# Kernel optimization log

Measured on AMD Instinct MI355X. Metric: run time of the kernel, lower is better.

Reference implementation:

```python
import jax, jax.numpy as jnp
import numpy as np

N_HEADS = 16
N_EMBD = 1024

def setup_inputs() -> dict:
    key = jax.random.key(0)
    k1, k2, k3, k4, k5 = jax.random.split(key, 5)
    B, T, C = 4, 2048, N_EMBD
    x = jax.random.normal(k1, (B, T, C), dtype=jnp.float32)
    # Linear weights stored as [in, out] (equivalent math to torch's x @ W.T + b)
    W_attn = jax.random.normal(k2, (C, 3 * C), dtype=jnp.float32) * 0.02
    b_attn = jax.random.normal(k3, (3 * C,), dtype=jnp.float32) * 0.02
    W_proj = jax.random.normal(k4, (C, C), dtype=jnp.float32) * 0.02
    b_proj = jax.random.normal(k5, (C,), dtype=jnp.float32) * 0.02
    return {"x": x, "W_attn": W_attn, "b_attn": b_attn, "W_proj": W_proj, "b_proj": b_proj}

def reference(x, W_attn, b_attn, W_proj, b_proj):
    B, T, C = x.shape
    H = N_HEADS
    D = C // H
    scale = 1.0 / jnp.sqrt(jnp.asarray(D, dtype=x.dtype))
    # fused QKV projection
    qkv = x @ W_attn + b_attn                      # [B, T, 3C]
    q, k, v = jnp.split(qkv, 3, axis=-1)           # each [B, T, C]
    q = q.reshape(B, T, H, D)
    k = k.reshape(B, T, H, D)
    v = v.reshape(B, T, H, D)
    # non-causal SDPA
    scores = jnp.einsum('bqhd,bkhd->bhqk', q, k) * scale  # [B, H, T, T]
    attn = jax.nn.softmax(scores, axis=-1)
    y = jnp.einsum('bhqk,bkhd->bqhd', attn, v)     # [B, T, H, D]
    y = y.reshape(B, T, C)
    return y @ W_proj + b_proj
```

## Files before the change

### kernel.cpp

```cpp
#include <hip/hip_runtime.h>

typedef short s16x8 __attribute__((ext_vector_type(8)));
typedef short s16x4 __attribute__((ext_vector_type(4)));
typedef float f32x4 __attribute__((ext_vector_type(4)));

__device__ __forceinline__ unsigned short f2bf(float f) {
  unsigned u = __float_as_uint(f);
  u += 0x7fffu + ((u >> 16) & 1u);
  return (unsigned short)(u >> 16);
}
__device__ __forceinline__ float bf2f(unsigned short h) {
  return __uint_as_float(((unsigned)h) << 16);
}

__device__ __forceinline__ f32x4 mfma16_bf16(s16x4 a, s16x4 b, f32x4 c) {
#if __has_builtin(__builtin_amdgcn_mfma_f32_16x16x16bf16_1k)
  return __builtin_amdgcn_mfma_f32_16x16x16bf16_1k(a, b, c, 0, 0, 0);
#else
  asm volatile("v_mfma_f32_16x16x16_bf16 %0, %1, %2, %0" : "+v"(c) : "v"(a), "v"(b));
  return c;
#endif
}

#define GLOAD_LDS16(g, l)                                          \
  __builtin_amdgcn_global_load_lds(                                \
      (const __attribute__((address_space(1))) void*)(g),          \
      (__attribute__((address_space(3))) void*)(l), 16, 0, 0)


__global__ __launch_bounds__(256) void cvt_x_bf16(const float* __restrict__ in,
                                                  unsigned short* __restrict__ out) {
  int i = (blockIdx.x * 256 + threadIdx.x) * 4;
  float4 v = *(const float4*)(in + i);
  ushort4 o;
  o.x = f2bf(v.x); o.y = f2bf(v.y); o.z = f2bf(v.z); o.w = f2bf(v.w);
  *(ushort4*)(out + i) = o;
}

__global__ __launch_bounds__(256) void transpose_w(const float* __restrict__ W,
                                                   unsigned short* __restrict__ Wt,
                                                   int R, int C) {
  __shared__ float tile[32][33];
  int c0 = blockIdx.x * 32, r0 = blockIdx.y * 32;
  int x = threadIdx.x, ty = threadIdx.y;
  for (int yy = ty; yy < 32; yy += 8)
    tile[yy][x] = W[(size_t)(r0 + yy) * C + c0 + x];
  __syncthreads();
  for (int yy = ty; yy < 32; yy += 8)
    Wt[(size_t)(c0 + yy) * R + r0 + x] = f2bf(tile[x][yy]);
}

__global__ __launch_bounds__(256) void transpose_v(const unsigned short* __restrict__ qkv,
                                                   unsigned short* __restrict__ vt) {
  __shared__ unsigned short TT[32][72];
  const int bh = blockIdx.y;
  const int t0 = blockIdx.x * 32;
  const int b = bh >> 4, h = bh & 15;
  const int t = threadIdx.x;
  {
    int row = t >> 3, c8 = (t & 7) * 8;
    const unsigned short* src =
        qkv + (size_t)(b * 2048 + t0 + row) * 3072 + 2048 + h * 64 + c8;
    *(uint4*)&TT[row][c8] = *(const uint4*)src;
  }
  __syncthreads();
  {
    int drow = t >> 2, tc8 = (t & 3) * 8;
    uint4 val;
    unsigned short* vp = (unsigned short*)&val;
    for (int j = 0; j < 8; j++) vp[j] = TT[tc8 + j][drow];
    *(uint4*)(vt + (size_t)(bh * 64 + drow) * 2048 + t0 + tc8) = val;
  }
}


template <bool OUT_BF16>
__global__ __launch_bounds__(256) void gemm_bt(const unsigned short* __restrict__ A,
                                               const unsigned short* __restrict__ Bt,
                                               const float* __restrict__ bias,
                                               void* __restrict__ Cout,
                                               int M, int N, int K) {
  __shared__ __align__(16) unsigned short As[128 * 32];
  __shared__ __align__(16) unsigned short Bs[128 * 32];

  const int tid  = threadIdx.x;
  const int lane = tid & 63;
  const int w    = tid >> 6;
  const int lr   = lane & 15;
  const int quad = lane >> 4;
  const int wm   = (w >> 1) * 64;
  const int wn   = (w & 1) * 64;
  const int m0   = blockIdx.x * 128;
  const int n0   = blockIdx.y * 128;

  f32x4 acc[4][4];
  for (int i = 0; i < 4; i++)
    for (int j = 0; j < 4; j++)
      acc[i][j] = f32x4{0.f, 0.f, 0.f, 0.f};

  const int srow = tid >> 2;
  const int scb  = (tid & 3) * 8;
  const unsigned short* Ap = A  + (size_t)(m0 + srow) * K + scb;
  const unsigned short* Bp = Bt + (size_t)(n0 + srow) * K + scb;
  unsigned short* lA0 = As + w * 512;
  unsigned short* lA1 = As + 2048 + w * 512;
  unsigned short* lB0 = Bs + w * 512;
  unsigned short* lB1 = Bs + 2048 + w * 512;

  for (int kk = 0; kk < K; kk += 32) {
    __syncthreads();
    GLOAD_LDS16(Ap + kk, lA0);
    GLOAD_LDS16(Ap + (size_t)64 * K + kk, lA1);
    GLOAD_LDS16(Bp + kk, lB0);
    GLOAD_LDS16(Bp + (size_t)64 * K + kk, lB1);
    __syncthreads();

    s16x8 af[4], bf[4];
    for (int i = 0; i < 4; i++) af[i] = *(const s16x8*)&As[(wm + i * 16 + lr) * 32 + quad * 8];
    for (int j = 0; j < 4; j++) bf[j] = *(const s16x8*)&Bs[(wn + j * 16 + lr) * 32 + quad * 8];
    for (int i = 0; i < 4; i++)
      for (int j = 0; j < 4; j++)
        acc[i][j] = __builtin_amdgcn_mfma_f32_16x16x32_bf16(af[i], bf[j], acc[i][j], 0, 0, 0);
  }

  for (int j = 0; j < 4; j++) {
    int col = n0 + wn + j * 16 + lr;
    float bc = bias[col];
    for (int i = 0; i < 4; i++) {
      int rowb = m0 + wm + i * 16 + quad * 4;
      for (int r = 0; r < 4; r++) {
        float v = acc[i][j][r] + bc;
        if (OUT_BF16)
          ((unsigned short*)Cout)[(size_t)(rowb + r) * N + col] = f2bf(v);
        else
          ((float*)Cout)[(size_t)(rowb + r) * N + col] = v;
      }
    }
  }
}


__global__ __launch_bounds__(256, 4) void attn_flash(const unsigned short* __restrict__ qkv,
                                                     const unsigned short* __restrict__ vt,
                                                     unsigned short* __restrict__ y) {
  const int T = 2048, C3 = 3072;
  const int bh = blockIdx.x & 63;
  const int qt = blockIdx.x >> 6;
  const int b  = bh >> 4;
  const int h  = bh & 15;
  const int q0 = qt * 128;

  const int tid  = threadIdx.x;
  const int lane = tid & 63;
  const int w    = tid >> 6;
  const int lr   = lane & 15;
  const int quad = lane >> 4;

  __shared__ __align__(16) unsigned short Ks[64][64];
  __shared__ __align__(16) unsigned short Vs[64][64];

  s16x8 qf[2][2];
  const float QSC = 0.18033688f;
  for (int j = 0; j < 2; j++)
    for (int c = 0; c < 2; c++) {
      const unsigned short* qp =
          qkv + (size_t)(b * T + q0 + w * 32 + j * 16 + lr) * C3 + h * 64 + c * 32 + quad * 8;
      s16x8 t = *(const s16x8*)qp;
      s16x8 o;
      for (int e = 0; e < 8; e++)
        o[e] = (short)f2bf(bf2f((unsigned short)t[e]) * QSC);
      qf[j][c] = o;
    }

  f32x4 O[2][4];
  for (int j = 0; j < 2; j++)
    for (int dt = 0; dt < 4; dt++) O[j][dt] = f32x4{0.f, 0.f, 0.f, 0.f};
  float l[2] = {0.f, 0.f};

  const int srow = tid >> 3;
  const int sc8  = (tid & 7) * 8;
  const int scb  = sc8 * 2;
  const unsigned short* kbase = qkv + (size_t)(b * T) * C3 + 1024 + (size_t)h * 64;
  const unsigned short* vbase = vt + (size_t)(bh * 64) * 2048;
  char* KsB = (char*)Ks;
  char* VsB = (char*)Vs;
  const int rswz = (lr & 7) << 4;

  for (int kt = 0; kt < 32; kt++) {
    const int k0 = kt * 64;
    __syncthreads();
    for (int rr = 0; rr < 64; rr += 32) {
      int row = srow + rr;
      int sw  = scb ^ ((row & 7) << 4);
      *(uint4*)(KsB + row * 128 + sw) =
          *(const uint4*)(kbase + (size_t)(k0 + row) * C3 + sc8);
      *(uint4*)(VsB + row * 128 + sw) =
          *(const uint4*)(vbase + (size_t)row * 2048 + k0 + sc8);
    }
    __syncthreads();

    for (int i = 0; i < 4; i++) {
      const char* krow = KsB + (i * 16 + lr) * 128;
      s16x8 kf0 = *(const s16x8*)(krow + ((quad * 16) ^ rswz));
      s16x8 kf1 = *(const s16x8*)(krow + ((64 + quad * 16) ^ rswz));
      s16x4 vf[4];
      for (int dt = 0; dt < 4; dt++)
        vf[dt] = *(const s16x4*)(VsB + (dt * 16 + lr) * 128 + ((i * 32 + quad * 8) ^ rswz));

      for (int j = 0; j < 2; j++) {
        f32x4 S = f32x4{0.f, 0.f, 0.f, 0.f};
        S = __builtin_amdgcn_mfma_f32_16x16x32_bf16(kf0, qf[j][0], S, 0, 0, 0);
        S = __builtin_amdgcn_mfma_f32_16x16x32_bf16(kf1, qf[j][1], S, 0, 0, 0);
        float p0 = __builtin_amdgcn_exp2f(S[0]);
        float p1 = __builtin_amdgcn_exp2f(S[1]);
        float p2 = __builtin_amdgcn_exp2f(S[2]);
        float p3 = __builtin_amdgcn_exp2f(S[3]);
        l[j] += (p0 + p1) + (p2 + p3);
        unsigned u0 = __float_as_uint(p0) + 0x8000u;
        unsigned u1 = __float_as_uint(p1) + 0x8000u;
        unsigned u2 = __float_as_uint(p2) + 0x8000u;
        unsigned u3 = __float_as_uint(p3) + 0x8000u;
        union { unsigned u[2]; s16x4 v; } pk;
        pk.u[0] = __builtin_amdgcn_perm(u1, u0, 0x07060302u);
        pk.u[1] = __builtin_amdgcn_perm(u3, u2, 0x07060302u);
        for (int dt = 0; dt < 4; dt++)
          O[j][dt] = mfma16_bf16(pk.v, vf[dt], O[j][dt]);
      }
    }
  }

  for (int j = 0; j < 2; j++) {
    float s = l[j];
    s += __shfl_xor(s, 16, 64);
    s += __shfl_xor(s, 32, 64);
    l[j] = 1.f / s;
  }
  for (int j = 0; j < 2; j++) {
    float inv[4];
    for (int r = 0; r < 4; r++) inv[r] = __shfl(l[j], quad * 4 + r, 64);
    for (int dt = 0; dt < 4; dt++) {
      int col = h * 64 + dt * 16 + lr;
      for (int r = 0; r < 4; r++) {
        int row = b * T + q0 + w * 32 + j * 16 + quad * 4 + r;
        y[(size_t)row * 1024 + col] = f2bf(O[j][dt][r] * inv[r]);
      }
    }
  }
}


extern "C" void kernel_launch(void* const* d_in, const int* in_sizes, int n_in,
                              void* d_out, int out_size, void* d_ws, size_t ws_size,
                              hipStream_t stream) {
  const float* x  = (const float*)d_in[0];
  const float* Wa = (const float*)d_in[1];
  const float* ba = (const float*)d_in[2];
  const float* Wp = (const float*)d_in[3];
  const float* bp = (const float*)d_in[4];
  float* out = (float*)d_out;

  char* ws = (char*)d_ws;
  unsigned short* xb  = (unsigned short*)ws;
  unsigned short* Wat = (unsigned short*)(ws + 16777216);
  unsigned short* Wpt = (unsigned short*)(ws + 23068672);
  unsigned short* qkv = (unsigned short*)(ws + 25165824);
  unsigned short* vtr = (unsigned short*)(ws + 75497472);

  cvt_x_bf16<<<8192, 256, 0, stream>>>(x, xb);
  transpose_w<<<dim3(96, 32), dim3(32, 8), 0, stream>>>(Wa, Wat, 1024, 3072);
  transpose_w<<<dim3(32, 32), dim3(32, 8), 0, stream>>>(Wp, Wpt, 1024, 1024);

  gemm_bt<true><<<dim3(64, 24), 256, 0, stream>>>(xb, Wat, ba, qkv, 8192, 3072, 1024);

  transpose_v<<<dim3(64, 64), 256, 0, stream>>>(qkv, vtr);

  attn_flash<<<1024, 256, 0, stream>>>(qkv, vtr, xb);

  gemm_bt<false><<<dim3(64, 8), 256, 0, stream>>>(xb, Wpt, bp, out, 8192, 1024, 1024);
}
```

Baseline: 291.6 us.

## Use 16x16x32 MFMA for PV and compute row sums via MFMA with ones

```diff
diff --git a/kernel.cpp b/kernel.cpp
--- a/kernel.cpp
+++ b/kernel.cpp
@@ -11,15 +11,6 @@
 }
 __device__ __forceinline__ float bf2f(unsigned short h) {
   return __uint_as_float(((unsigned)h) << 16);
-}
-
-__device__ __forceinline__ f32x4 mfma16_bf16(s16x4 a, s16x4 b, f32x4 c) {
-#if __has_builtin(__builtin_amdgcn_mfma_f32_16x16x16bf16_1k)
-  return __builtin_amdgcn_mfma_f32_16x16x16bf16_1k(a, b, c, 0, 0, 0);
-#else
-  asm volatile("v_mfma_f32_16x16x16_bf16 %0, %1, %2, %0" : "+v"(c) : "v"(a), "v"(b));
-  return c;
-#endif
 }
 
 #define GLOAD_LDS16(g, l)                                          \
@@ -172,10 +163,15 @@
       qf[j][c] = o;
     }
 
+  s16x8 ones;
+  for (int e = 0; e < 8; e++) ones[e] = (short)0x3F80;
+
   f32x4 O[2][4];
-  for (int j = 0; j < 2; j++)
+  f32x4 Lacc[2];
+  for (int j = 0; j < 2; j++) {
     for (int dt = 0; dt < 4; dt++) O[j][dt] = f32x4{0.f, 0.f, 0.f, 0.f};
-  float l[2] = {0.f, 0.f};
+    Lacc[j] = f32x4{0.f, 0.f, 0.f, 0.f};
+  }
 
   const int srow = tid >> 3;
   const int sc8  = (tid & 7) * 8;
@@ -191,58 +187,61 @@
     __syncthreads();
     for (int rr = 0; rr < 64; rr += 32) {
       int row = srow + rr;
+      int r32 = row & 31;
+      int key = (row & ~31) | (((r32 & 12) << 1) | ((r32 >> 4) << 2) | (r32 & 3));
       int sw  = scb ^ ((row & 7) << 4);
       *(uint4*)(KsB + row * 128 + sw) =
-          *(const uint4*)(kbase + (size_t)(k0 + row) * C3 + sc8);
+          *(const uint4*)(kbase + (size_t)(k0 + key) * C3 + sc8);
       *(uint4*)(VsB + row * 128 + sw) =
           *(const uint4*)(vbase + (size_t)row * 2048 + k0 + sc8);
     }
     __syncthreads();
 
-    for (int i = 0; i < 4; i++) {
-      const char* krow = KsB + (i * 16 + lr) * 128;
-      s16x8 kf0 = *(const s16x8*)(krow + ((quad * 16) ^ rswz));
-      s16x8 kf1 = *(const s16x8*)(krow + ((64 + quad * 16) ^ rswz));
-      s16x4 vf[4];
+    for (int ch = 0; ch < 2; ch++) {
+      const char* krowA = KsB + (ch * 32 + lr) * 128;
+      const char* krowB = KsB + (ch * 32 + 16 + lr) * 128;
+      s16x8 kA0 = *(const s16x8*)(krowA + ((quad * 16) ^ rswz));
+      s16x8 kA1 = *(const s16x8*)(krowA + ((64 + quad * 16) ^ rswz));
+      s16x8 kB0 = *(const s16x8*)(krowB + ((quad * 16) ^ rswz));
+      s16x8 kB1 = *(const s16x8*)(krowB + ((64 + quad * 16) ^ rswz));
+      s16x8 vf[4];
       for (int dt = 0; dt < 4; dt++)
-        vf[dt] = *(const s16x4*)(VsB + (dt * 16 + lr) * 128 + ((i * 32 + quad * 8) ^ rswz));
+        vf[dt] = *(const s16x8*)(VsB + (dt * 16 + lr) * 128 + ((ch * 64 + quad * 16) ^ rswz));
 
       for (int j = 0; j < 2; j++) {
-        f32x4 S = f32x4{0.f, 0.f, 0.f, 0.f};
-        S = __builtin_amdgcn_mfma_f32_16x16x32_bf16(kf0, qf[j][0], S, 0, 0, 0);
-        S = __builtin_amdgcn_mfma_f32_16x16x32_bf16(kf1, qf[j][1], S, 0, 0, 0);
-        float p0 = __builtin_amdgcn_exp2f(S[0]);
-        float p1 = __builtin_amdgcn_exp2f(S[1]);
-        float p2 = __builtin_amdgcn_exp2f(S[2]);
-        float p3 = __builtin_amdgcn_exp2f(S[3]);
-        l[j] += (p0 + p1) + (p2 + p3);
-        unsigned u0 = __float_as_uint(p0) + 0x8000u;
-        unsigned u1 = __float_as_uint(p1) + 0x8000u;
-        unsigned u2 = __float_as_uint(p2) + 0x8000u;
-        unsigned u3 = __float_as_uint(p3) + 0x8000u;
-        union { unsigned u[2]; s16x4 v; } pk;
+        f32x4 Sa = f32x4{0.f, 0.f, 0.f, 0.f};
+        f32x4 Sb = f32x4{0.f, 0.f, 0.f, 0.f};
+        Sa = __builtin_amdgcn_mfma_f32_16x16x32_bf16(kA0, qf[j][0], Sa, 0, 0, 0);
+        Sa = __builtin_amdgcn_mfma_f32_16x16x32_bf16(kA1, qf[j][1], Sa, 0, 0, 0);
+        Sb = __builtin_amdgcn_mfma_f32_16x16x32_bf16(kB0, qf[j][0], Sb, 0, 0, 0);
+        Sb = __builtin_amdgcn_mfma_f32_16x16x32_bf16(kB1, qf[j][1], Sb, 0, 0, 0);
+        unsigned u0 = __float_as_uint(__builtin_amdgcn_exp2f(Sa[0])) + 0x8000u;
+        unsigned u1 = __float_as_uint(__builtin_amdgcn_exp2f(Sa[1])) + 0x8000u;
+        unsigned u2 = __float_as_uint(__builtin_amdgcn_exp2f(Sa[2])) + 0x8000u;
+        unsigned u3 = __float_as_uint(__builtin_amdgcn_exp2f(Sa[3])) + 0x8000u;
+        unsigned u4 = __float_as_uint(__builtin_amdgcn_exp2f(Sb[0])) + 0x8000u;
+        unsigned u5 = __float_as_uint(__builtin_amdgcn_exp2f(Sb[1])) + 0x8000u;
+        unsigned u6 = __float_as_uint(__builtin_amdgcn_exp2f(Sb[2])) + 0x8000u;
+        unsigned u7 = __float_as_uint(__builtin_amdgcn_exp2f(Sb[3])) + 0x8000u;
+        union { unsigned u[4]; s16x8 v; } pk;
         pk.u[0] = __builtin_amdgcn_perm(u1, u0, 0x07060302u);
         pk.u[1] = __builtin_amdgcn_perm(u3, u2, 0x07060302u);
+        pk.u[2] = __builtin_amdgcn_perm(u5, u4, 0x07060302u);
+        pk.u[3] = __builtin_amdgcn_perm(u7, u6, 0x07060302u);
+        Lacc[j] = __builtin_amdgcn_mfma_f32_16x16x32_bf16(pk.v, ones, Lacc[j], 0, 0, 0);
         for (int dt = 0; dt < 4; dt++)
-          O[j][dt] = mfma16_bf16(pk.v, vf[dt], O[j][dt]);
+          O[j][dt] = __builtin_amdgcn_mfma_f32_16x16x32_bf16(pk.v, vf[dt], O[j][dt], 0, 0, 0);
       }
     }
   }
 
   for (int j = 0; j < 2; j++) {
-    float s = l[j];
-    s += __shfl_xor(s, 16, 64);
-    s += __shfl_xor(s, 32, 64);
-    l[j] = 1.f / s;
-  }
-  for (int j = 0; j < 2; j++) {
-    float inv[4];
-    for (int r = 0; r < 4; r++) inv[r] = __shfl(l[j], quad * 4 + r, 64);
-    for (int dt = 0; dt < 4; dt++) {
-      int col = h * 64 + dt * 16 + lr;
-      for (int r = 0; r < 4; r++) {
-        int row = b * T + q0 + w * 32 + j * 16 + quad * 4 + r;
-        y[(size_t)row * 1024 + col] = f2bf(O[j][dt][r] * inv[r]);
+    for (int r = 0; r < 4; r++) {
+      float inv = 1.f / Lacc[j][r];
+      int row = b * T + q0 + w * 32 + j * 16 + quad * 4 + r;
+      for (int dt = 0; dt < 4; dt++) {
+        int col = h * 64 + dt * 16 + lr;
+        y[(size_t)row * 1024 + col] = f2bf(O[j][dt][r] * inv);
       }
     }
   }
```

Measured after the change: 283.9 us. -2.6%, faster.
